# Kernel optimization log

Measured on AMD Instinct MI355X. Metric: run time of the kernel, lower is better.

## Reference

```python
import jax, jax.numpy as jnp
import numpy as np

U, I, D, L = 100000, 100000, 64, 50
B, T = 4096, 100


def setup_inputs() -> dict:
    key = jax.random.key(0)
    ks = jax.random.split(key, 12)
    inp = {}
    inp["item_seq"] = jax.random.randint(ks[0], (B, L), 0, I, dtype=jnp.int64 if jax.config.jax_enable_x64 else jnp.int32)
    inp["user_ids"] = jax.random.randint(ks[1], (B,), 0, U, dtype=jnp.int32)
    inp["items_to_predict"] = jax.random.randint(ks[2], (B, T), 0, I, dtype=jnp.int32)
    # parameters (match torch inits: N(0, 1/d) embeddings, xavier gates, zero b2)
    inp["user_emb_table"] = jax.random.normal(ks[3], (U, D), jnp.float32) / D
    inp["item_emb_table"] = jax.random.normal(ks[4], (I, D), jnp.float32) / D
    lin_s = float(np.sqrt(1.0 / D))
    inp["fg_item_W"] = jax.random.uniform(ks[5], (D, D), jnp.float32, -lin_s, lin_s)
    inp["fg_item_b"] = jax.random.uniform(ks[6], (D,), jnp.float32, -lin_s, lin_s)
    inp["fg_user_W"] = jax.random.uniform(ks[7], (D, D), jnp.float32, -lin_s, lin_s)
    inp["fg_user_b"] = jax.random.uniform(ks[8], (D,), jnp.float32, -lin_s, lin_s)
    xg1 = float(np.sqrt(6.0 / (D + 1)))
    xg2 = float(np.sqrt(6.0 / (D + L)))
    inp["instance_gate_item"] = jax.random.uniform(ks[9], (D, 1), jnp.float32, -xg1, xg1)
    inp["instance_gate_user"] = jax.random.uniform(ks[10], (D, L), jnp.float32, -xg2, xg2)
    W2 = jax.random.normal(ks[11], (I, D), jnp.float32) / D
    inp["W2_table"] = W2.at[0].set(0.0)  # padding_idx=0
    inp["b2_table"] = jnp.zeros((I, 1), jnp.float32)
    return inp


def reference(item_seq, user_ids, items_to_predict, user_emb_table, item_emb_table,
              fg_item_W, fg_item_b, fg_user_W, fg_user_b,
              instance_gate_item, instance_gate_user, W2_table, b2_table):
    item_embs = item_emb_table[item_seq]          # [B, L, D]
    user_emb = user_emb_table[user_ids]           # [B, D]
    # feature gating
    gate = jax.nn.sigmoid(item_embs @ fg_item_W + fg_item_b
                          + (user_emb @ fg_user_W + fg_user_b)[:, None, :])
    gated_item = item_embs * gate                 # [B, L, D]
    # instance gating
    instance_score = jax.nn.sigmoid(
        jnp.einsum('bld,d->bl', gated_item, instance_gate_item[:, 0])
        + user_emb @ instance_gate_user)          # [B, L]
    union_out = jnp.sum(gated_item * instance_score[..., None], axis=1)
    union_out = union_out / jnp.sum(instance_score, axis=1, keepdims=True)  # [B, D]
    # scoring (for_pred=False branch)
    w2 = W2_table[items_to_predict]               # [B, T, D]
    b2 = b2_table[items_to_predict][..., 0]       # [B, T]
    res = b2 + jnp.einsum('btd,bd->bt', w2, user_emb)
    res = res + jnp.einsum('btd,bd->bt', w2, union_out)
    # rel_score: sum_l item_embs @ w2^T == (sum_l item_embs) . w2
    res = res + jnp.einsum('bd,btd->bt', item_embs.sum(axis=1), w2)
    return res
```

## Files before the change

### kernel.cpp

```cpp
#include <hip/hip_runtime.h>

#define D_ 64
#define L_ 50
#define B_ 4096
#define T_ 100
#define SP 65
#define RS 72

typedef __attribute__((ext_vector_type(8))) short  short8;
typedef __attribute__((ext_vector_type(4))) float  float4v;
typedef __attribute__((ext_vector_type(4))) unsigned short ushort4v;

__device__ __forceinline__ float sigmoidf_(float x) {
    return 1.0f / (1.0f + __expf(-x));
}
__device__ __forceinline__ unsigned short f2bf(float x) {
    unsigned u = __builtin_bit_cast(unsigned, x);
    return (unsigned short)((u + 0x7fffu + ((u >> 16) & 1u)) >> 16);
}
__device__ __forceinline__ float bf2f(unsigned short s) {
    return __builtin_bit_cast(float, (unsigned)s << 16);
}

__global__ __launch_bounds__(256) void hgn_transpose_w(
    const float* __restrict__ fg_item_W, unsigned short* __restrict__ wbT)
{
    const int i = blockIdx.x * 256 + threadIdx.x;
    const int k = i >> 6, c = i & 63;
    wbT[c * 64 + k] = f2bf(fg_item_W[i]);
}

__global__ __launch_bounds__(256) void hgn_fused_kernel(
    const int* __restrict__ item_seq,
    const int* __restrict__ user_ids,
    const int* __restrict__ items_to_predict,
    const float* __restrict__ user_emb_table,
    const float* __restrict__ item_emb_table,
    const unsigned short* __restrict__ wbT,
    const float* __restrict__ fg_item_b,
    const float* __restrict__ fg_user_W,
    const float* __restrict__ fg_user_b,
    const float* __restrict__ ig_item,
    const float* __restrict__ ig_user,
    const float* __restrict__ W2,
    const float* __restrict__ b2,
    float* __restrict__ out)
{
    __shared__ unsigned short eb_sh[64 * RS];
    __shared__ float part_sh[L_ * SP];
    __shared__ __align__(16) float u_sh[D_];
    __shared__ __align__(16) float v_sh[D_];
    __shared__ float gb_sh[D_];
    __shared__ float s_sh[L_];
    __shared__ float bp_sh[2][64];
    __shared__ float esum_sh[D_];
    __shared__ int   idx_sh[L_];

    const int t    = threadIdx.x;
    const int lane = t & 63;
    const int wave = t >> 6;
    const int b    = blockIdx.x;

    if (t < L_) idx_sh[t] = item_seq[b * L_ + t];
    if (t >= 64 && t < 128) {
        const int uid = user_ids[b];
        u_sh[t - 64] = user_emb_table[(size_t)uid * D_ + (t - 64)];
    }
    __syncthreads();

    if (wave == 3) {
        float g0 = fg_item_b[lane], g1 = fg_user_b[lane], g2 = 0.f, g3 = 0.f;
#pragma unroll
        for (int k = 0; k < D_; k += 4) {
            g0 = fmaf(u_sh[k + 0], fg_user_W[(k + 0) * D_ + lane], g0);
            g1 = fmaf(u_sh[k + 1], fg_user_W[(k + 1) * D_ + lane], g1);
            g2 = fmaf(u_sh[k + 2], fg_user_W[(k + 2) * D_ + lane], g2);
            g3 = fmaf(u_sh[k + 3], fg_user_W[(k + 3) * D_ + lane], g3);
        }
        gb_sh[lane] = (g0 + g1) + (g2 + g3);
    } else {
        for (int i = t; i < L_ * 16; i += 192) {
            const int l = i >> 4, qd = i & 15;
            const float4 r = ((const float4*)(item_emb_table + (size_t)idx_sh[l] * D_))[qd];
            ushort4v o = { f2bf(r.x), f2bf(r.y), f2bf(r.z), f2bf(r.w) };
            *(ushort4v*)&eb_sh[l * RS + qd * 4] = o;
        }
    }
    __syncthreads();

    {
        const int m = lane & 15, q = lane >> 4;
        const int arow = 16 * wave + m;
        const short8 a0 = *(const short8*)&eb_sh[arow * RS + q * 8];
        const short8 a1 = *(const short8*)&eb_sh[arow * RS + 32 + q * 8];
#pragma unroll
        for (int n = 0; n < 4; ++n) {
            const int col = 16 * n + m;
            const short8 b0 = *(const short8*)&wbT[col * 64 + q * 8];
            const short8 b1 = *(const short8*)&wbT[col * 64 + 32 + q * 8];
            float4v acc = {0.f, 0.f, 0.f, 0.f};
            acc = __builtin_amdgcn_mfma_f32_16x16x32_bf16(a0, b0, acc, 0, 0, 0);
            acc = __builtin_amdgcn_mfma_f32_16x16x32_bf16(a1, b1, acc, 0, 0, 0);
            const float gbc = gb_sh[col];
#pragma unroll
            for (int r = 0; r < 4; ++r) {
                const int l = 16 * wave + q * 4 + r;
                if (l < L_) {
                    const float e = bf2f(eb_sh[l * RS + col]);
                    part_sh[l * SP + col] = e * sigmoidf_(acc[r] + gbc);
                }
            }
        }
    }
    __syncthreads();

    if (wave < 2) {
        if (lane < L_) {
            const int d0 = 32 * wave;
            float p0 = 0.f, p1 = 0.f, p2 = 0.f, p3 = 0.f;
#pragma unroll
            for (int j = 0; j < 32; j += 4) {
                const int d = d0 + j;
                p0 = fmaf(part_sh[lane * SP + d + 0], ig_item[d + 0], p0);
                p1 = fmaf(part_sh[lane * SP + d + 1], ig_item[d + 1], p1);
                p2 = fmaf(part_sh[lane * SP + d + 2], ig_item[d + 2], p2);
                p3 = fmaf(part_sh[lane * SP + d + 3], ig_item[d + 3], p3);
                p0 = fmaf(u_sh[d + 0], ig_user[(d + 0) * L_ + lane], p0);
                p1 = fmaf(u_sh[d + 1], ig_user[(d + 1) * L_ + lane], p1);
                p2 = fmaf(u_sh[d + 2], ig_user[(d + 2) * L_ + lane], p2);
                p3 = fmaf(u_sh[d + 3], ig_user[(d + 3) * L_ + lane], p3);
            }
            bp_sh[wave][lane] = (p0 + p1) + (p2 + p3);
        }
    } else if (wave == 2) {
        float e0 = 0.f, e1 = 0.f;
#pragma unroll
        for (int l = 0; l < L_; l += 2) {
            e0 += bf2f(eb_sh[l * RS + lane]);
            e1 += bf2f(eb_sh[(l + 1) * RS + lane]);
        }
        esum_sh[lane] = e0 + e1;
    }
    __syncthreads();

    if (wave == 0) {
        if (lane < L_) s_sh[lane] = sigmoidf_(bp_sh[0][lane] + bp_sh[1][lane]);
        float a0 = 0.f, a1 = 0.f, ss = 0.f;
        for (int l = 0; l < L_; l += 2) {
            const float sA = s_sh[l], sB = s_sh[l + 1];
            a0 = fmaf(part_sh[l * SP + lane], sA, a0);
            a1 = fmaf(part_sh[(l + 1) * SP + lane], sB, a1);
            ss += sA + sB;
        }
        v_sh[lane] = u_sh[lane] + (a0 + a1) / ss + esum_sh[lane];
    }
    __syncthreads();

    if (t < 2 * T_) {
        const int tt = t >> 1, half = t & 1;
        const int idx = items_to_predict[b * T_ + tt];
        const float* wrow  = W2 + (size_t)idx * D_ + half * 32;
        const float* vhalf = v_sh + half * 32;
        float r0 = 0.f, r1 = 0.f, r2 = 0.f, r3 = 0.f;
#pragma unroll
        for (int kk = 0; kk < 8; ++kk) {
            const float4 w4 = ((const float4*)wrow)[kk];
            const float4 v4 = ((const float4*)vhalf)[kk];
            r0 = fmaf(v4.x, w4.x, r0);
            r1 = fmaf(v4.y, w4.y, r1);
            r2 = fmaf(v4.z, w4.z, r2);
            r3 = fmaf(v4.w, w4.w, r3);
        }
        float r = (r0 + r1) + (r2 + r3);
        r += __shfl_xor(r, 1, 64);
        if (half == 0) out[b * T_ + tt] = r + b2[idx];
    }
}

extern "C" void kernel_launch(void* const* d_in, const int* in_sizes, int n_in,
                              void* d_out, int out_size, void* d_ws, size_t ws_size,
                              hipStream_t stream) {
    const int*   item_seq   = (const int*)d_in[0];
    const int*   user_ids   = (const int*)d_in[1];
    const int*   items_pred = (const int*)d_in[2];
    const float* uet        = (const float*)d_in[3];
    const float* iet        = (const float*)d_in[4];
    const float* fgiW       = (const float*)d_in[5];
    const float* fgib       = (const float*)d_in[6];
    const float* fguW       = (const float*)d_in[7];
    const float* fgub       = (const float*)d_in[8];
    const float* igi        = (const float*)d_in[9];
    const float* igu        = (const float*)d_in[10];
    const float* W2         = (const float*)d_in[11];
    const float* b2t        = (const float*)d_in[12];

    unsigned short* wbT = (unsigned short*)d_ws;

    hgn_transpose_w<<<16, 256, 0, stream>>>(fgiW, wbT);
    hgn_fused_kernel<<<B_, 256, 0, stream>>>(
        item_seq, user_ids, items_pred, uet, iet,
        wbT, fgib, fguW, fgub, igi, igu, W2, b2t, (float*)d_out);
}
```

Baseline: 165.5 us.

## Keep gated items in MFMA registers and reduce instance gating via shuffles

Removes the part_sh shared-memory staging of gated item embeddings. The instance-gate score, sigmoid, weighted sum, and item-embedding sum are now computed directly from the MFMA accumulator registers using cross-lane shuffles and a small per-wave reduction buffer, which drops one barrier phase and the serial loops over L. It also moves the user-side instance gate dot product into the otherwise idle wave 3, unrolls the embedding gather into independent loads, and prefetches items_to_predict and b2 at kernel start. The trade-offs are higher register pressure and more shuffle instructions.

```diff
diff --git a/kernel.cpp b/kernel.cpp
--- a/kernel.cpp
+++ b/kernel.cpp
@@ -4,7 +4,6 @@
 #define L_ 50
 #define B_ 4096
 #define T_ 100
-#define SP 65
 #define RS 72
 
 typedef __attribute__((ext_vector_type(8))) short  short8;
@@ -47,14 +46,13 @@
     float* __restrict__ out)
 {
     __shared__ unsigned short eb_sh[64 * RS];
-    __shared__ float part_sh[L_ * SP];
     __shared__ __align__(16) float u_sh[D_];
     __shared__ __align__(16) float v_sh[D_];
     __shared__ float gb_sh[D_];
-    __shared__ float s_sh[L_];
-    __shared__ float bp_sh[2][64];
-    __shared__ float esum_sh[D_];
-    __shared__ int   idx_sh[L_];
+    __shared__ float usl_sh[D_];
+    __shared__ __align__(16) float red_sh[4][128];
+    __shared__ float ss_sh[4];
+    __shared__ int   idx_sh[D_];
 
     const int t    = threadIdx.x;
     const int lane = t & 63;
@@ -65,6 +63,12 @@
     if (t >= 64 && t < 128) {
         const int uid = user_ids[b];
         u_sh[t - 64] = user_emb_table[(size_t)uid * D_ + (t - 64)];
+    }
+    int   idxt  = 0;
+    float b2pre = 0.f;
+    if (t < 2 * T_) {
+        idxt  = items_to_predict[b * T_ + (t >> 1)];
+        b2pre = b2[idxt];
     }
     __syncthreads();
 
@@ -78,12 +82,40 @@
             g3 = fmaf(u_sh[k + 3], fg_user_W[(k + 3) * D_ + lane], g3);
         }
         gb_sh[lane] = (g0 + g1) + (g2 + g3);
+        if (lane < L_) {
+            float us0 = 0.f, us1 = 0.f;
+#pragma unroll
+            for (int d = 0; d < D_; d += 2) {
+                us0 = fmaf(u_sh[d + 0], ig_user[(d + 0) * L_ + lane], us0);
+                us1 = fmaf(u_sh[d + 1], ig_user[(d + 1) * L_ + lane], us1);
+            }
+            usl_sh[lane] = us0 + us1;
+        }
     } else {
-        for (int i = t; i < L_ * 16; i += 192) {
-            const int l = i >> 4, qd = i & 15;
-            const float4 r = ((const float4*)(item_emb_table + (size_t)idx_sh[l] * D_))[qd];
-            ushort4v o = { f2bf(r.x), f2bf(r.y), f2bf(r.z), f2bf(r.w) };
-            *(ushort4v*)&eb_sh[l * RS + qd * 4] = o;
+        const int base = wave * 64 + lane;
+        const int c0 = base, c1 = base + 192, c2 = base + 384, c3 = base + 576,
+                  c4 = base + 768;
+        const bool tail = (base < 32);
+        float4 r0 = ((const float4*)(item_emb_table + (size_t)idx_sh[c0 >> 4] * D_))[c0 & 15];
+        float4 r1 = ((const float4*)(item_emb_table + (size_t)idx_sh[c1 >> 4] * D_))[c1 & 15];
+        float4 r2 = ((const float4*)(item_emb_table + (size_t)idx_sh[c2 >> 4] * D_))[c2 & 15];
+        float4 r3 = ((const float4*)(item_emb_table + (size_t)idx_sh[c3 >> 4] * D_))[c3 & 15];
+        float4 r4 = {0.f, 0.f, 0.f, 0.f};
+        if (tail)
+            r4 = ((const float4*)(item_emb_table + (size_t)idx_sh[c4 >> 4] * D_))[c4 & 15];
+        {
+            ushort4v o0 = { f2bf(r0.x), f2bf(r0.y), f2bf(r0.z), f2bf(r0.w) };
+            *(ushort4v*)&eb_sh[(c0 >> 4) * RS + (c0 & 15) * 4] = o0;
+            ushort4v o1 = { f2bf(r1.x), f2bf(r1.y), f2bf(r1.z), f2bf(r1.w) };
+            *(ushort4v*)&eb_sh[(c1 >> 4) * RS + (c1 & 15) * 4] = o1;
+            ushort4v o2 = { f2bf(r2.x), f2bf(r2.y), f2bf(r2.z), f2bf(r2.w) };
+            *(ushort4v*)&eb_sh[(c2 >> 4) * RS + (c2 & 15) * 4] = o2;
+            ushort4v o3 = { f2bf(r3.x), f2bf(r3.y), f2bf(r3.z), f2bf(r3.w) };
+            *(ushort4v*)&eb_sh[(c3 >> 4) * RS + (c3 & 15) * 4] = o3;
+            if (tail) {
+                ushort4v o4 = { f2bf(r4.x), f2bf(r4.y), f2bf(r4.z), f2bf(r4.w) };
+                *(ushort4v*)&eb_sh[(c4 >> 4) * RS + (c4 & 15) * 4] = o4;
+            }
         }
     }
     __syncthreads();
@@ -93,6 +125,10 @@
         const int arow = 16 * wave + m;
         const short8 a0 = *(const short8*)&eb_sh[arow * RS + q * 8];
         const short8 a1 = *(const short8*)&eb_sh[arow * RS + 32 + q * 8];
+
+        float gi[4][4];
+        float ep[4];
+        float sp[4] = {0.f, 0.f, 0.f, 0.f};
 #pragma unroll
         for (int n = 0; n < 4; ++n) {
             const int col = 16 * n + m;
@@ -102,64 +138,74 @@
             acc = __builtin_amdgcn_mfma_f32_16x16x32_bf16(a0, b0, acc, 0, 0, 0);
             acc = __builtin_amdgcn_mfma_f32_16x16x32_bf16(a1, b1, acc, 0, 0, 0);
             const float gbc = gb_sh[col];
+            const float igc = ig_item[col];
+            float epn = 0.f;
 #pragma unroll
             for (int r = 0; r < 4; ++r) {
                 const int l = 16 * wave + q * 4 + r;
+                float gv = 0.f;
                 if (l < L_) {
                     const float e = bf2f(eb_sh[l * RS + col]);
-                    part_sh[l * SP + col] = e * sigmoidf_(acc[r] + gbc);
+                    gv  = e * sigmoidf_(acc[r] + gbc);
+                    epn += e;
+                    sp[r] = fmaf(gv, igc, sp[r]);
                 }
+                gi[n][r] = gv;
             }
-        }
-    }
-    __syncthreads();
-
-    if (wave < 2) {
-        if (lane < L_) {
-            const int d0 = 32 * wave;
-            float p0 = 0.f, p1 = 0.f, p2 = 0.f, p3 = 0.f;
-#pragma unroll
-            for (int j = 0; j < 32; j += 4) {
-                const int d = d0 + j;
-                p0 = fmaf(part_sh[lane * SP + d + 0], ig_item[d + 0], p0);
-                p1 = fmaf(part_sh[lane * SP + d + 1], ig_item[d + 1], p1);
-                p2 = fmaf(part_sh[lane * SP + d + 2], ig_item[d + 2], p2);
-                p3 = fmaf(part_sh[lane * SP + d + 3], ig_item[d + 3], p3);
-                p0 = fmaf(u_sh[d + 0], ig_user[(d + 0) * L_ + lane], p0);
-                p1 = fmaf(u_sh[d + 1], ig_user[(d + 1) * L_ + lane], p1);
-                p2 = fmaf(u_sh[d + 2], ig_user[(d + 2) * L_ + lane], p2);
-                p3 = fmaf(u_sh[d + 3], ig_user[(d + 3) * L_ + lane], p3);
-            }
-            bp_sh[wave][lane] = (p0 + p1) + (p2 + p3);
-        }
-    } else if (wave == 2) {
-        float e0 = 0.f, e1 = 0.f;
-#pragma unroll
-        for (int l = 0; l < L_; l += 2) {
-            e0 += bf2f(eb_sh[l * RS + lane]);
-            e1 += bf2f(eb_sh[(l + 1) * RS + lane]);
-        }
-        esum_sh[lane] = e0 + e1;
+            ep[n] = epn;
+        }
+
+#pragma unroll
+        for (int r = 0; r < 4; ++r) {
+            float v = sp[r];
+            v += __shfl_xor(v, 1);  v += __shfl_xor(v, 2);
+            v += __shfl_xor(v, 4);  v += __shfl_xor(v, 8);
+            sp[r] = v;
+        }
+        float s[4];
+        float ssr = 0.f;
+#pragma unroll
+        for (int r = 0; r < 4; ++r) {
+            const int l = 16 * wave + q * 4 + r;
+            const float sv = (l < L_) ? sigmoidf_(sp[r] + usl_sh[l]) : 0.f;
+            s[r] = sv;
+            ssr += sv;
+        }
+        ssr += __shfl_xor(ssr, 16);  ssr += __shfl_xor(ssr, 32);
+        if (lane == 0) ss_sh[wave] = ssr;
+
+        float unA[4], enA[4];
+#pragma unroll
+        for (int n = 0; n < 4; ++n) {
+            float un = fmaf(gi[n][0], s[0], fmaf(gi[n][1], s[1],
+                        fmaf(gi[n][2], s[2], gi[n][3] * s[3])));
+            un += __shfl_xor(un, 16);  un += __shfl_xor(un, 32);
+            float en = ep[n];
+            en += __shfl_xor(en, 16);  en += __shfl_xor(en, 32);
+            unA[n] = un;  enA[n] = en;
+        }
+        const float unq = (q == 0) ? unA[0] : (q == 1) ? unA[1] : (q == 2) ? unA[2] : unA[3];
+        const float enq = (q == 0) ? enA[0] : (q == 1) ? enA[1] : (q == 2) ? enA[2] : enA[3];
+        float2 pr;  pr.x = unq;  pr.y = enq;
+        *(float2*)&red_sh[wave][(16 * q + m) * 2] = pr;
     }
     __syncthreads();
 
     if (wave == 0) {
-        if (lane < L_) s_sh[lane] = sigmoidf_(bp_sh[0][lane] + bp_sh[1][lane]);
-        float a0 = 0.f, a1 = 0.f, ss = 0.f;
-        for (int l = 0; l < L_; l += 2) {
-            const float sA = s_sh[l], sB = s_sh[l + 1];
-            a0 = fmaf(part_sh[l * SP + lane], sA, a0);
-            a1 = fmaf(part_sh[(l + 1) * SP + lane], sB, a1);
-            ss += sA + sB;
-        }
-        v_sh[lane] = u_sh[lane] + (a0 + a1) / ss + esum_sh[lane];
+        float un = 0.f, en = 0.f;
+#pragma unroll
+        for (int w = 0; w < 4; ++w) {
+            const float2 pr = *(const float2*)&red_sh[w][lane * 2];
+            un += pr.x;  en += pr.y;
+        }
+        const float ss = (ss_sh[0] + ss_sh[1]) + (ss_sh[2] + ss_sh[3]);
+        v_sh[lane] = u_sh[lane] + un / ss + en;
     }
     __syncthreads();
 
     if (t < 2 * T_) {
-        const int tt = t >> 1, half = t & 1;
-        const int idx = items_to_predict[b * T_ + tt];
-        const float* wrow  = W2 + (size_t)idx * D_ + half * 32;
+        const int half = t & 1;
+        const float* wrow  = W2 + (size_t)idxt * D_ + half * 32;
         const float* vhalf = v_sh + half * 32;
         float r0 = 0.f, r1 = 0.f, r2 = 0.f, r3 = 0.f;
 #pragma unroll
@@ -173,7 +219,7 @@
         }
         float r = (r0 + r1) + (r2 + r3);
         r += __shfl_xor(r, 1, 64);
-        if (half == 0) out[b * T_ + tt] = r + b2[idx];
+        if (half == 0) out[b * T_ + (t >> 1)] = r + b2pre;
     }
 }
 
```

After: 163.8 us. Within noise of the previous version (-1.0%).
